# Kernel tuning notes

Measured on AMD Instinct MI355X. Metric: run time of the kernel, lower is better.

The kernel has to match this reference:

```python
import jax, jax.numpy as jnp
import numpy as np

F_BANKS = 8
D_IN = 592
FILTER_W = 5.0
BATCH = 8192


def _init(k, shape, fan_in):
    bound = 1.0 / np.sqrt(fan_in)
    return jax.random.uniform(k, shape, jnp.float32, -bound, bound)


def setup_inputs() -> dict:
    key = jax.random.key(0)
    ks = jax.random.split(key, 11)
    F = F_BANKS
    return {
        "x": jax.random.normal(ks[0], (BATCH, D_IN), jnp.float32),
        # per-bank Conv1d(1->3,k=3) and Conv1d(3->1,k=3), stacked over banks
        "conv1_w": _init(ks[1], (F, 3, 1, 3), 1 * 3),
        "conv1_b": _init(ks[2], (F, 3), 1 * 3),
        "conv2_w": _init(ks[3], (F, 1, 3, 3), 3 * 3),
        "conv2_b": _init(ks[4], (F, 1), 3 * 3),
        # per-bank MLP 36 -> 20 -> 10 -> 1
        "lin1_w": _init(ks[5], (F, 20, 36), 36),
        "lin1_b": _init(ks[6], (F, 20), 36),
        "lin2_w": _init(ks[7], (F, 10, 20), 20),
        "lin2_b": _init(ks[8], (F, 10), 20),
        "lin3_w": _init(ks[9], (F, 1, 10), 10),
        "lin3_b": _init(ks[10], (F, 1), 10),
    }


def _conv1d(x, w, b, stride):
    # x: [B, C_in, L], w: [C_out, C_in, K]
    y = jax.lax.conv_general_dilated(x, w, (stride,), "VALID",
                                     dimension_numbers=("NCH", "OIH", "NCH"))
    return y + b[None, :, None]


def _maxpool3s2(x):
    # MaxPool1d(kernel=3, stride=2) over last axis of [B, C, L]
    return jax.lax.reduce_window(x, -jnp.inf, jax.lax.max, (1, 1, 3), (1, 1, 2), "VALID")


def reference(x, conv1_w, conv1_b, conv2_w, conv2_b,
              lin1_w, lin1_b, lin2_w, lin2_b, lin3_w, lin3_b):
    B, D = x.shape
    f = jnp.arange(D, dtype=x.dtype)  # frequency grid [D]
    inv_2w2 = 1.0 / (2.0 * FILTER_W * FILTER_W)

    filtered_sum = jnp.zeros_like(x)
    H_list, xf_list, xs_list, f0_list = [], [], [], []
    for i in range(F_BANKS):
        x_aux = x - filtered_sum  # residual signal fed to bank i
        xs_list.append(x_aux)
        # conv bank: [B,1,592] -> [B,3,295] -> [B,3,147] -> [B,1,73] -> [B,1,36]
        h = x_aux[:, None, :]
        h = jax.nn.relu(_maxpool3s2(_conv1d(h, conv1_w[i], conv1_b[i], 2)))
        h = jax.nn.relu(_maxpool3s2(_conv1d(h, conv2_w[i], conv2_b[i], 2)))
        h = h[:, 0, :]  # squeeze(1) -> [B, 36]
        # linear bank: 36 -> 20 -> 10 -> 1 with sigmoid head
        h = jax.nn.relu(h @ lin1_w[i].T + lin1_b[i])
        h = jax.nn.relu(h @ lin2_w[i].T + lin2_b[i])
        h = jax.nn.sigmoid(h @ lin3_w[i].T + lin3_b[i])  # [B, 1]
        f0 = D * h  # center frequency per sample, [B, 1]
        # Gaussian filter per sample, vectorized over the batch (replaces per-row loop)
        H = jnp.exp(-jnp.square(f[None, :] - f0) * inv_2w2)  # [B, D]
        xf = x_aux * H
        filtered_sum = filtered_sum + xf
        H_list.append(H)
        xf_list.append(xf)
        f0_list.append(f0)
    return (jnp.stack(H_list), jnp.stack(xf_list), jnp.stack(xs_list), jnp.stack(f0_list))
```

## Files before the change

### kernel.cpp

```cpp
#include <hip/hip_runtime.h>
#include <math.h>

#define BATCH  8192
#define D_IN   592
#define FBANKS 8
#define P1     147
#define P2     36
#define P1PAD  152
#define NW     4

#define WAVE_SYNC() do { __builtin_amdgcn_wave_barrier(); asm volatile("" ::: "memory"); } while (0)


__global__ __launch_bounds__(256, 6) void fb_kernel(
    const float* __restrict__ x,
    const float* __restrict__ c1w, const float* __restrict__ c1b,
    const float* __restrict__ c2w, const float* __restrict__ c2b,
    const float* __restrict__ l1w, const float* __restrict__ l1b,
    const float* __restrict__ l2w, const float* __restrict__ l2b,
    const float* __restrict__ l3w, const float* __restrict__ l3b,
    float* __restrict__ outH, float* __restrict__ outXF,
    float* __restrict__ outXS, float* __restrict__ outF0)
{
    __shared__ __align__(16) float s_xa[NW][D_IN];
    __shared__ __align__(16) float s_p1[NW][3][P1PAD];
    __shared__ __align__(16) float s_p2[NW][40];
    __shared__ __align__(16) float s_l1o[NW][20];

    const int tid  = threadIdx.x;
    const int wave = tid >> 6;
    const int lane = tid & 63;
    const int row  = blockIdx.x * NW + wave;

    float* xa = s_xa[wave];
    {
        const float* xrow = x + (size_t)row * D_IN;
        for (int i = lane; i < 148; i += 64) {
            *(float4*)&xa[4 * i] = *(const float4*)&xrow[4 * i];
        }
    }
    WAVE_SYNC();

    const float negc2 = -0.028853900817779268f;

    for (int bank = 0; bank < FBANKS; ++bank) {
        float w1[3][3], b1[3], w2[3][3];
        #pragma unroll
        for (int c = 0; c < 3; ++c) {
            b1[c] = c1b[bank * 3 + c];
            #pragma unroll
            for (int k = 0; k < 3; ++k) {
                w1[c][k] = c1w[bank * 9 + c * 3 + k];
                w2[c][k] = c2w[bank * 9 + c * 3 + k];
            }
        }
        const float b2 = c2b[bank];

        for (int p = lane; p < P1; p += 64) {
            float4 a = *(const float4*)&xa[4 * p];
            float4 b = *(const float4*)&xa[4 * p + 4];
            float xv0 = a.x, xv1 = a.y, xv2 = a.z, xv3 = a.w;
            float xv4 = b.x, xv5 = b.y, xv6 = b.z;
            #pragma unroll
            for (int c = 0; c < 3; ++c) {
                float v0 = w1[c][0] * xv0 + w1[c][1] * xv1 + w1[c][2] * xv2;
                float v1 = w1[c][0] * xv2 + w1[c][1] * xv3 + w1[c][2] * xv4;
                float v2 = w1[c][0] * xv4 + w1[c][1] * xv5 + w1[c][2] * xv6;
                float m  = fmaxf(fmaxf(v0, v1), v2) + b1[c];
                s_p1[wave][c][p] = fmaxf(m, 0.0f);
            }
        }
        WAVE_SYNC();

        if (lane < P2) {
            const int q = lane;
            float acc0 = b2, acc1 = b2, acc2 = b2;
            #pragma unroll
            for (int c = 0; c < 3; ++c) {
                const float* r = s_p1[wave][c];
                float4 a = *(const float4*)&r[4 * q];
                float4 b = *(const float4*)&r[4 * q + 4];
                float v0 = a.x, v1 = a.y, v2 = a.z, v3 = a.w, v4 = b.x, v5 = b.y, v6 = b.z;
                acc0 += w2[c][0] * v0 + w2[c][1] * v1 + w2[c][2] * v2;
                acc1 += w2[c][0] * v2 + w2[c][1] * v3 + w2[c][2] * v4;
                acc2 += w2[c][0] * v4 + w2[c][1] * v5 + w2[c][2] * v6;
            }
            float mm = fmaxf(fmaxf(acc0, acc1), acc2);
            s_p2[wave][q] = fmaxf(mm, 0.0f);
        }
        WAVE_SYNC();

        if (lane < 20) {
            const float4* wr = (const float4*)(l1w + bank * 720 + lane * 36);
            float acc = l1b[bank * 20 + lane];
            #pragma unroll
            for (int k = 0; k < 9; ++k) {
                float4 w = wr[k];
                float4 v = *(const float4*)&s_p2[wave][4 * k];
                acc += w.x * v.x + w.y * v.y + w.z * v.z + w.w * v.w;
            }
            s_l1o[wave][lane] = fmaxf(acc, 0.0f);
        }
        WAVE_SYNC();

        float part = 0.0f;
        if (lane < 10) {
            const float4* wr = (const float4*)(l2w + bank * 200 + lane * 20);
            float acc = l2b[bank * 10 + lane];
            #pragma unroll
            for (int k = 0; k < 5; ++k) {
                float4 w = wr[k];
                float4 v = *(const float4*)&s_l1o[wave][4 * k];
                acc += w.x * v.x + w.y * v.y + w.z * v.z + w.w * v.w;
            }
            part = fmaxf(acc, 0.0f) * l3w[bank * 10 + lane];
        }
        part += __shfl_xor(part, 1);
        part += __shfl_xor(part, 2);
        part += __shfl_xor(part, 4);
        part += __shfl_xor(part, 8);
        float acc3 = __uint_as_float(__builtin_amdgcn_readfirstlane(__float_as_uint(part)))
                   + l3b[bank];
        float sig  = 1.0f / (1.0f + __expf(-acc3));
        float f0v  = (float)D_IN * sig;
        if (lane == 0) outF0[(size_t)bank * BATCH + row] = f0v;

        const size_t base = ((size_t)bank * BATCH + row) * D_IN;
        for (int i = lane; i < 148; i += 64) {
            float4 xv = *(const float4*)&xa[4 * i];
            float d0 = (float)(4 * i) - f0v;
            float d1 = d0 + 1.0f;
            float d2 = d0 + 2.0f;
            float d3 = d0 + 3.0f;
            float4 Hv, xf, xn;
            Hv.x = __builtin_amdgcn_exp2f(d0 * d0 * negc2);
            Hv.y = __builtin_amdgcn_exp2f(d1 * d1 * negc2);
            Hv.z = __builtin_amdgcn_exp2f(d2 * d2 * negc2);
            Hv.w = __builtin_amdgcn_exp2f(d3 * d3 * negc2);
            xf.x = xv.x * Hv.x;  xf.y = xv.y * Hv.y;
            xf.z = xv.z * Hv.z;  xf.w = xv.w * Hv.w;
            xn.x = xv.x - xf.x;  xn.y = xv.y - xf.y;
            xn.z = xv.z - xf.z;  xn.w = xv.w - xf.w;
            *(float4*)&outXS[base + 4 * i] = xv;
            *(float4*)&outH [base + 4 * i] = Hv;
            *(float4*)&outXF[base + 4 * i] = xf;
            if (bank != FBANKS - 1)
                *(float4*)&xa[4 * i] = xn;
        }
        WAVE_SYNC();
    }
}

extern "C" void kernel_launch(void* const* d_in, const int* in_sizes, int n_in,
                              void* d_out, int out_size, void* d_ws, size_t ws_size,
                              hipStream_t stream) {
    const float* x   = (const float*)d_in[0];
    const float* c1w = (const float*)d_in[1];
    const float* c1b = (const float*)d_in[2];
    const float* c2w = (const float*)d_in[3];
    const float* c2b = (const float*)d_in[4];
    const float* l1w = (const float*)d_in[5];
    const float* l1b = (const float*)d_in[6];
    const float* l2w = (const float*)d_in[7];
    const float* l2b = (const float*)d_in[8];
    const float* l3w = (const float*)d_in[9];
    const float* l3b = (const float*)d_in[10];

    float* out = (float*)d_out;
    const size_t plane = (size_t)FBANKS * BATCH * D_IN;
    float* outH  = out;
    float* outXF = out + plane;
    float* outXS = out + 2 * plane;
    float* outF0 = out + 3 * plane;

    dim3 grid(BATCH / NW);
    dim3 block(256);
    fb_kernel<<<grid, block, 0, stream>>>(x, c1w, c1b, c2w, c2b,
                                          l1w, l1b, l2w, l2b, l3w, l3b,
                                          outH, outXF, outXS, outF0);
}
```

Measured before the change: 501.3 us.

## Defer all output stores to a single pass after computing every bank's f0

The per-bank loop now computes only f0 and updates the residual in shared memory, with no global writes of H, XF or XS. After all banks finish, one final loop reloads x from global memory and recomputes the filter chain for all eight banks in registers, writing every output in a single burst. The goal is to separate the compute-heavy sequential conv/MLP phase from the bandwidth-bound store phase so stores come in one contiguous stream. In exchange, exp2 and residual arithmetic is done twice, and results could differ slightly if the recomputed residual chain does not match the shared-memory one.

```diff
diff --git a/kernel.cpp b/kernel.cpp
--- a/kernel.cpp
+++ b/kernel.cpp
@@ -8,6 +8,7 @@
 #define P2     36
 #define P1PAD  152
 #define NW     4
+#define PLANE  ((size_t)BATCH * D_IN)
 
 #define WAVE_SYNC() do { __builtin_amdgcn_wave_barrier(); asm volatile("" ::: "memory"); } while (0)
 
@@ -26,6 +27,7 @@
     __shared__ __align__(16) float s_p1[NW][3][P1PAD];
     __shared__ __align__(16) float s_p2[NW][40];
     __shared__ __align__(16) float s_l1o[NW][20];
+    __shared__ __align__(16) float s_f0[NW][8];
 
     const int tid  = threadIdx.x;
     const int wave = tid >> 6;
@@ -33,11 +35,9 @@
     const int row  = blockIdx.x * NW + wave;
 
     float* xa = s_xa[wave];
-    {
-        const float* xrow = x + (size_t)row * D_IN;
-        for (int i = lane; i < 148; i += 64) {
-            *(float4*)&xa[4 * i] = *(const float4*)&xrow[4 * i];
-        }
+    const float* xrow = x + (size_t)row * D_IN;
+    for (int i = lane; i < 148; i += 64) {
+        *(float4*)&xa[4 * i] = *(const float4*)&xrow[4 * i];
     }
     WAVE_SYNC();
 
@@ -123,31 +123,58 @@
                    + l3b[bank];
         float sig  = 1.0f / (1.0f + __expf(-acc3));
         float f0v  = (float)D_IN * sig;
-        if (lane == 0) outF0[(size_t)bank * BATCH + row] = f0v;
-
-        const size_t base = ((size_t)bank * BATCH + row) * D_IN;
-        for (int i = lane; i < 148; i += 64) {
-            float4 xv = *(const float4*)&xa[4 * i];
-            float d0 = (float)(4 * i) - f0v;
-            float d1 = d0 + 1.0f;
-            float d2 = d0 + 2.0f;
-            float d3 = d0 + 3.0f;
-            float4 Hv, xf, xn;
+        if (lane == 0) {
+            s_f0[wave][bank] = f0v;
+            outF0[(size_t)bank * BATCH + row] = f0v;
+        }
+
+        if (bank < FBANKS - 1) {
+            for (int i = lane; i < 148; i += 64) {
+                float4 xv = *(const float4*)&xa[4 * i];
+                float d0 = (float)(4 * i) - f0v;
+                float d1 = d0 + 1.0f, d2 = d0 + 2.0f, d3 = d0 + 3.0f;
+                float4 Hv, xf;
+                Hv.x = __builtin_amdgcn_exp2f(d0 * d0 * negc2);
+                Hv.y = __builtin_amdgcn_exp2f(d1 * d1 * negc2);
+                Hv.z = __builtin_amdgcn_exp2f(d2 * d2 * negc2);
+                Hv.w = __builtin_amdgcn_exp2f(d3 * d3 * negc2);
+                xf.x = xv.x * Hv.x;  xf.y = xv.y * Hv.y;
+                xf.z = xv.z * Hv.z;  xf.w = xv.w * Hv.w;
+                float4 xn;
+                xn.x = xv.x - xf.x;  xn.y = xv.y - xf.y;
+                xn.z = xv.z - xf.z;  xn.w = xv.w - xf.w;
+                *(float4*)&xa[4 * i] = xn;
+            }
+        }
+        WAVE_SYNC();
+    }
+
+    float f0s[FBANKS];
+    #pragma unroll
+    for (int b = 0; b < FBANKS; ++b) f0s[b] = s_f0[wave][b];
+    const size_t rowoff = (size_t)row * D_IN;
+
+    for (int i = lane; i < 148; i += 64) {
+        float4 xv = *(const float4*)&xrow[4 * i];
+        const float e0 = (float)(4 * i);
+        #pragma unroll
+        for (int b = 0; b < FBANKS; ++b) {
+            const size_t off = (size_t)b * PLANE + rowoff + 4 * i;
+            float d0 = e0 - f0s[b];
+            float d1 = d0 + 1.0f, d2 = d0 + 2.0f, d3 = d0 + 3.0f;
+            float4 Hv, xf;
             Hv.x = __builtin_amdgcn_exp2f(d0 * d0 * negc2);
             Hv.y = __builtin_amdgcn_exp2f(d1 * d1 * negc2);
             Hv.z = __builtin_amdgcn_exp2f(d2 * d2 * negc2);
             Hv.w = __builtin_amdgcn_exp2f(d3 * d3 * negc2);
             xf.x = xv.x * Hv.x;  xf.y = xv.y * Hv.y;
             xf.z = xv.z * Hv.z;  xf.w = xv.w * Hv.w;
-            xn.x = xv.x - xf.x;  xn.y = xv.y - xf.y;
-            xn.z = xv.z - xf.z;  xn.w = xv.w - xf.w;
-            *(float4*)&outXS[base + 4 * i] = xv;
-            *(float4*)&outH [base + 4 * i] = Hv;
-            *(float4*)&outXF[base + 4 * i] = xf;
-            if (bank != FBANKS - 1)
-                *(float4*)&xa[4 * i] = xn;
-        }
-        WAVE_SYNC();
+            *(float4*)&outXS[off] = xv;
+            *(float4*)&outH [off] = Hv;
+            *(float4*)&outXF[off] = xf;
+            xv.x -= xf.x;  xv.y -= xf.y;
+            xv.z -= xf.z;  xv.w -= xf.w;
+        }
     }
 }
 
```

Result: slower. 550.8 us (+9.9%).

## Stage H in LDS and write whole-block contiguous outputs with nontemporal stores

Applied to the files above, without the earlier changes.

Each wave now computes its Gaussian filter row into a new shared buffer. After a block-wide barrier, all 256 threads cooperatively write the four rows' contiguous XS/H/XF spans (4 adjacent rows form one contiguous region per bank) using nontemporal stores. The goal is more coalesced, cache-bypassing streaming writes for this store-bound kernel. In exchange it adds two __syncthreads per bank, extra LDS traffic and footprint, and lowers the occupancy hint from 6 to 5.

```diff
diff --git a/kernel.cpp b/kernel.cpp
--- a/kernel.cpp
+++ b/kernel.cpp
@@ -12,7 +12,14 @@
 #define WAVE_SYNC() do { __builtin_amdgcn_wave_barrier(); asm volatile("" ::: "memory"); } while (0)
 
 
-__global__ __launch_bounds__(256, 6) void fb_kernel(
+typedef float f4v __attribute__((ext_vector_type(4)));
+static __device__ __forceinline__ void nt_store4(float* p, float a, float b,
+                                                 float c, float d) {
+    f4v t = {a, b, c, d};
+    __builtin_nontemporal_store(t, (f4v*)p);
+}
+
+__global__ __launch_bounds__(256, 5) void fb_kernel(
     const float* __restrict__ x,
     const float* __restrict__ c1w, const float* __restrict__ c1b,
     const float* __restrict__ c2w, const float* __restrict__ c2b,
@@ -23,6 +30,7 @@
     float* __restrict__ outXS, float* __restrict__ outF0)
 {
     __shared__ __align__(16) float s_xa[NW][D_IN];
+    __shared__ __align__(16) float s_oH[NW][D_IN];
     __shared__ __align__(16) float s_p1[NW][3][P1PAD];
     __shared__ __align__(16) float s_p2[NW][40];
     __shared__ __align__(16) float s_l1o[NW][20];
@@ -31,13 +39,12 @@
     const int wave = tid >> 6;
     const int lane = tid & 63;
     const int row  = blockIdx.x * NW + wave;
+    const size_t blkrow = (size_t)blockIdx.x * NW;
 
     float* xa = s_xa[wave];
-    {
-        const float* xrow = x + (size_t)row * D_IN;
-        for (int i = lane; i < 148; i += 64) {
-            *(float4*)&xa[4 * i] = *(const float4*)&xrow[4 * i];
-        }
+    const float* xrow = x + (size_t)row * D_IN;
+    for (int i = lane; i < 148; i += 64) {
+        *(float4*)&xa[4 * i] = *(const float4*)&xrow[4 * i];
     }
     WAVE_SYNC();
 
@@ -125,27 +132,84 @@
         float f0v  = (float)D_IN * sig;
         if (lane == 0) outF0[(size_t)bank * BATCH + row] = f0v;
 
-        const size_t base = ((size_t)bank * BATCH + row) * D_IN;
-        for (int i = lane; i < 148; i += 64) {
-            float4 xv = *(const float4*)&xa[4 * i];
-            float d0 = (float)(4 * i) - f0v;
-            float d1 = d0 + 1.0f;
-            float d2 = d0 + 2.0f;
-            float d3 = d0 + 3.0f;
-            float4 Hv, xf, xn;
+        float4 xn0, xn1, xn2 = {0.f, 0.f, 0.f, 0.f};
+        {
+            float4 xv = *(const float4*)&xa[4 * lane];
+            float d0 = (float)(4 * lane) - f0v;
+            float4 Hv;
             Hv.x = __builtin_amdgcn_exp2f(d0 * d0 * negc2);
-            Hv.y = __builtin_amdgcn_exp2f(d1 * d1 * negc2);
-            Hv.z = __builtin_amdgcn_exp2f(d2 * d2 * negc2);
-            Hv.w = __builtin_amdgcn_exp2f(d3 * d3 * negc2);
-            xf.x = xv.x * Hv.x;  xf.y = xv.y * Hv.y;
-            xf.z = xv.z * Hv.z;  xf.w = xv.w * Hv.w;
-            xn.x = xv.x - xf.x;  xn.y = xv.y - xf.y;
-            xn.z = xv.z - xf.z;  xn.w = xv.w - xf.w;
-            *(float4*)&outXS[base + 4 * i] = xv;
-            *(float4*)&outH [base + 4 * i] = Hv;
-            *(float4*)&outXF[base + 4 * i] = xf;
-            if (bank != FBANKS - 1)
-                *(float4*)&xa[4 * i] = xn;
+            Hv.y = __builtin_amdgcn_exp2f((d0 + 1.f) * (d0 + 1.f) * negc2);
+            Hv.z = __builtin_amdgcn_exp2f((d0 + 2.f) * (d0 + 2.f) * negc2);
+            Hv.w = __builtin_amdgcn_exp2f((d0 + 3.f) * (d0 + 3.f) * negc2);
+            *(float4*)&s_oH[wave][4 * lane] = Hv;
+            xn0.x = xv.x - xv.x * Hv.x;  xn0.y = xv.y - xv.y * Hv.y;
+            xn0.z = xv.z - xv.z * Hv.z;  xn0.w = xv.w - xv.w * Hv.w;
+        }
+        {
+            const int e = 4 * (64 + lane);
+            float4 xv = *(const float4*)&xa[e];
+            float d0 = (float)e - f0v;
+            float4 Hv;
+            Hv.x = __builtin_amdgcn_exp2f(d0 * d0 * negc2);
+            Hv.y = __builtin_amdgcn_exp2f((d0 + 1.f) * (d0 + 1.f) * negc2);
+            Hv.z = __builtin_amdgcn_exp2f((d0 + 2.f) * (d0 + 2.f) * negc2);
+            Hv.w = __builtin_amdgcn_exp2f((d0 + 3.f) * (d0 + 3.f) * negc2);
+            *(float4*)&s_oH[wave][e] = Hv;
+            xn1.x = xv.x - xv.x * Hv.x;  xn1.y = xv.y - xv.y * Hv.y;
+            xn1.z = xv.z - xv.z * Hv.z;  xn1.w = xv.w - xv.w * Hv.w;
+        }
+        if (lane < 20) {
+            const int e = 4 * (128 + lane);
+            float4 xv = *(const float4*)&xa[e];
+            float d0 = (float)e - f0v;
+            float4 Hv;
+            Hv.x = __builtin_amdgcn_exp2f(d0 * d0 * negc2);
+            Hv.y = __builtin_amdgcn_exp2f((d0 + 1.f) * (d0 + 1.f) * negc2);
+            Hv.z = __builtin_amdgcn_exp2f((d0 + 2.f) * (d0 + 2.f) * negc2);
+            Hv.w = __builtin_amdgcn_exp2f((d0 + 3.f) * (d0 + 3.f) * negc2);
+            *(float4*)&s_oH[wave][e] = Hv;
+            xn2.x = xv.x - xv.x * Hv.x;  xn2.y = xv.y - xv.y * Hv.y;
+            xn2.z = xv.z - xv.z * Hv.z;  xn2.w = xv.w - xv.w * Hv.w;
+        }
+        __syncthreads();
+
+        {
+            const size_t base = ((size_t)bank * BATCH + blkrow) * D_IN;
+            const float* xf_ = &s_xa[0][0];
+            const float* hf_ = &s_oH[0][0];
+            {   const int u = tid;
+                float4 xv = *(const float4*)&xf_[4 * u];
+                float4 hv = *(const float4*)&hf_[4 * u];
+                nt_store4((float*)&outXS[base + 4 * u], xv.x, xv.y, xv.z, xv.w);
+                nt_store4((float*)&outH [base + 4 * u], hv.x, hv.y, hv.z, hv.w);
+                nt_store4((float*)&outXF[base + 4 * u], xv.x * hv.x, xv.y * hv.y,
+                                                        xv.z * hv.z, xv.w * hv.w);
+            }
+            {   const int u = tid + 256;
+                float4 xv = *(const float4*)&xf_[4 * u];
+                float4 hv = *(const float4*)&hf_[4 * u];
+                nt_store4((float*)&outXS[base + 4 * u], xv.x, xv.y, xv.z, xv.w);
+                nt_store4((float*)&outH [base + 4 * u], hv.x, hv.y, hv.z, hv.w);
+                nt_store4((float*)&outXF[base + 4 * u], xv.x * hv.x, xv.y * hv.y,
+                                                        xv.z * hv.z, xv.w * hv.w);
+            }
+            if (tid < 80) {
+                const int u = tid + 512;
+                float4 xv = *(const float4*)&xf_[4 * u];
+                float4 hv = *(const float4*)&hf_[4 * u];
+                nt_store4((float*)&outXS[base + 4 * u], xv.x, xv.y, xv.z, xv.w);
+                nt_store4((float*)&outH [base + 4 * u], hv.x, hv.y, hv.z, hv.w);
+                nt_store4((float*)&outXF[base + 4 * u], xv.x * hv.x, xv.y * hv.y,
+                                                        xv.z * hv.z, xv.w * hv.w);
+            }
+        }
+        __syncthreads();
+
+        if (bank < FBANKS - 1) {
+            *(float4*)&xa[4 * lane]        = xn0;
+            *(float4*)&xa[4 * (64 + lane)] = xn1;
+            if (lane < 20)
+                *(float4*)&xa[4 * (128 + lane)] = xn2;
         }
         WAVE_SYNC();
     }
```

Result: no change. 499.8 us (-0.3%).

## Split into compute-only chain kernel and streaming output writer kernel

Applied to the files above, without the earlier changes.

The fused kernel becomes two kernels. The first runs the conv/MLP chain per row and writes only f0, recomputing the residual in shared memory without storing the big planes. The second is a flat streaming kernel where each thread owns float4 chunks across all banks, recomputes the Gaussian filter and writes H, XF and XS with nontemporal stores. The aim is to decouple the latency-bound chain from the bandwidth-bound 465MB of output writes so stores can saturate HBM, at the cost of recomputing the exps and a second launch.

```diff
diff --git a/kernel.cpp b/kernel.cpp
--- a/kernel.cpp
+++ b/kernel.cpp
@@ -8,19 +8,26 @@
 #define P2     36
 #define P1PAD  152
 #define NW     4
+#define PLANE  ((size_t)BATCH * D_IN)
+
 
 #define WAVE_SYNC() do { __builtin_amdgcn_wave_barrier(); asm volatile("" ::: "memory"); } while (0)
 
-
-__global__ __launch_bounds__(256, 6) void fb_kernel(
+typedef float f4v __attribute__((ext_vector_type(4)));
+static __device__ __forceinline__ void nt_store4p(float* p, float a, float b,
+                                                  float c, float d) {
+    f4v t = {a, b, c, d};
+    __builtin_nontemporal_store(t, (f4v*)p);
+}
+
+__global__ __launch_bounds__(256, 8) void fb_chain(
     const float* __restrict__ x,
     const float* __restrict__ c1w, const float* __restrict__ c1b,
     const float* __restrict__ c2w, const float* __restrict__ c2b,
     const float* __restrict__ l1w, const float* __restrict__ l1b,
     const float* __restrict__ l2w, const float* __restrict__ l2b,
     const float* __restrict__ l3w, const float* __restrict__ l3b,
-    float* __restrict__ outH, float* __restrict__ outXF,
-    float* __restrict__ outXS, float* __restrict__ outF0)
+    float* __restrict__ outF0)
 {
     __shared__ __align__(16) float s_xa[NW][D_IN];
     __shared__ __align__(16) float s_p1[NW][3][P1PAD];
@@ -33,11 +40,9 @@
     const int row  = blockIdx.x * NW + wave;
 
     float* xa = s_xa[wave];
-    {
-        const float* xrow = x + (size_t)row * D_IN;
-        for (int i = lane; i < 148; i += 64) {
-            *(float4*)&xa[4 * i] = *(const float4*)&xrow[4 * i];
-        }
+    const float* xrow = x + (size_t)row * D_IN;
+    for (int i = lane; i < 148; i += 64) {
+        *(float4*)&xa[4 * i] = *(const float4*)&xrow[4 * i];
     }
     WAVE_SYNC();
 
@@ -125,29 +130,81 @@
         float f0v  = (float)D_IN * sig;
         if (lane == 0) outF0[(size_t)bank * BATCH + row] = f0v;
 
-        const size_t base = ((size_t)bank * BATCH + row) * D_IN;
-        for (int i = lane; i < 148; i += 64) {
-            float4 xv = *(const float4*)&xa[4 * i];
-            float d0 = (float)(4 * i) - f0v;
-            float d1 = d0 + 1.0f;
-            float d2 = d0 + 2.0f;
-            float d3 = d0 + 3.0f;
-            float4 Hv, xf, xn;
-            Hv.x = __builtin_amdgcn_exp2f(d0 * d0 * negc2);
-            Hv.y = __builtin_amdgcn_exp2f(d1 * d1 * negc2);
-            Hv.z = __builtin_amdgcn_exp2f(d2 * d2 * negc2);
-            Hv.w = __builtin_amdgcn_exp2f(d3 * d3 * negc2);
-            xf.x = xv.x * Hv.x;  xf.y = xv.y * Hv.y;
-            xf.z = xv.z * Hv.z;  xf.w = xv.w * Hv.w;
-            xn.x = xv.x - xf.x;  xn.y = xv.y - xf.y;
-            xn.z = xv.z - xf.z;  xn.w = xv.w - xf.w;
-            *(float4*)&outXS[base + 4 * i] = xv;
-            *(float4*)&outH [base + 4 * i] = Hv;
-            *(float4*)&outXF[base + 4 * i] = xf;
-            if (bank != FBANKS - 1)
+        if (bank < FBANKS - 1) {
+            for (int i = lane; i < 148; i += 64) {
+                float4 xv = *(const float4*)&xa[4 * i];
+                float d0 = (float)(4 * i) - f0v;
+                float h0 = __builtin_amdgcn_exp2f(d0 * d0 * negc2);
+                float h1 = __builtin_amdgcn_exp2f((d0 + 1.f) * (d0 + 1.f) * negc2);
+                float h2 = __builtin_amdgcn_exp2f((d0 + 2.f) * (d0 + 2.f) * negc2);
+                float h3 = __builtin_amdgcn_exp2f((d0 + 3.f) * (d0 + 3.f) * negc2);
+                float4 xn;
+                xn.x = xv.x - xv.x * h0;  xn.y = xv.y - xv.y * h1;
+                xn.z = xv.z - xv.z * h2;  xn.w = xv.w - xv.w * h3;
                 *(float4*)&xa[4 * i] = xn;
-        }
-        WAVE_SYNC();
+            }
+        }
+        WAVE_SYNC();
+    }
+}
+
+#define K2_BLOCKS 2048
+#define K2_GSZ    (K2_BLOCKS * 256)
+#define NUNITS    (BATCH * 148)
+
+static __device__ __forceinline__ void bank_step(float4& xa, float ebase, float f0v,
+                                                 float* pH, float* pXF, float* pXS) {
+    const float negc2 = -0.028853900817779268f;
+    float d0 = ebase - f0v;
+    float h0 = __builtin_amdgcn_exp2f(d0 * d0 * negc2);
+    float h1 = __builtin_amdgcn_exp2f((d0 + 1.f) * (d0 + 1.f) * negc2);
+    float h2 = __builtin_amdgcn_exp2f((d0 + 2.f) * (d0 + 2.f) * negc2);
+    float h3 = __builtin_amdgcn_exp2f((d0 + 3.f) * (d0 + 3.f) * negc2);
+    float xf0 = xa.x * h0, xf1 = xa.y * h1, xf2 = xa.z * h2, xf3 = xa.w * h3;
+    nt_store4p(pXS, xa.x, xa.y, xa.z, xa.w);
+    nt_store4p(pH,  h0, h1, h2, h3);
+    nt_store4p(pXF, xf0, xf1, xf2, xf3);
+    xa.x -= xf0;  xa.y -= xf1;  xa.z -= xf2;  xa.w -= xf3;
+}
+
+__global__ __launch_bounds__(256, 4) void fb_stream(
+    const float* __restrict__ x, const float* __restrict__ f0t,
+    float* __restrict__ outH, float* __restrict__ outXF,
+    float* __restrict__ outXS)
+{
+    const int gtid = blockIdx.x * 256 + threadIdx.x;
+    const int u0 = gtid;
+    const int u1 = gtid + K2_GSZ;
+    const int u2 = gtid + 2 * K2_GSZ;
+    const bool a2 = (u2 < NUNITS);
+
+    const int r0 = u0 / 148, i0 = u0 - 148 * r0;
+    const int r1 = u1 / 148, i1 = u1 - 148 * r1;
+    const int r2i = a2 ? u2 : 0;
+    const int r2 = r2i / 148, i2 = r2i - 148 * r2;
+
+    const float e0 = (float)(4 * i0);
+    const float e1 = (float)(4 * i1);
+    const float e2 = (float)(4 * i2);
+
+    float4 xa0 = *(const float4*)&x[(size_t)r0 * D_IN + 4 * i0];
+    float4 xa1 = *(const float4*)&x[(size_t)r1 * D_IN + 4 * i1];
+    float4 xa2 = *(const float4*)&x[(size_t)r2 * D_IN + 4 * i2];
+
+    const size_t o0 = (size_t)r0 * D_IN + 4 * i0;
+    const size_t o1 = (size_t)r1 * D_IN + 4 * i1;
+    const size_t o2 = (size_t)r2 * D_IN + 4 * i2;
+
+    #pragma unroll
+    for (int b = 0; b < FBANKS; ++b) {
+        const size_t sb = (size_t)b * PLANE;
+        const float f00 = f0t[b * BATCH + r0];
+        const float f01 = f0t[b * BATCH + r1];
+        const float f02 = f0t[b * BATCH + r2];
+        bank_step(xa0, e0, f00, &outH[sb + o0], &outXF[sb + o0], &outXS[sb + o0]);
+        bank_step(xa1, e1, f01, &outH[sb + o1], &outXF[sb + o1], &outXS[sb + o1]);
+        if (a2)
+            bank_step(xa2, e2, f02, &outH[sb + o2], &outXF[sb + o2], &outXS[sb + o2]);
     }
 }
 
@@ -173,9 +230,8 @@
     float* outXS = out + 2 * plane;
     float* outF0 = out + 3 * plane;
 
-    dim3 grid(BATCH / NW);
-    dim3 block(256);
-    fb_kernel<<<grid, block, 0, stream>>>(x, c1w, c1b, c2w, c2b,
-                                          l1w, l1b, l2w, l2b, l3w, l3b,
-                                          outH, outXF, outXS, outF0);
-}
+    fb_chain<<<dim3(BATCH / NW), dim3(256), 0, stream>>>(
+        x, c1w, c1b, c2w, c2b, l1w, l1b, l2w, l2b, l3w, l3b, outF0);
+    fb_stream<<<dim3(K2_BLOCKS), dim3(256), 0, stream>>>(
+        x, outF0, outH, outXF, outXS);
+}
```

New measurement: 527.0 us. 1.05x slower.
